# Performance work log

Hardware: AMD Instinct MI355X
Metric: run time of the kernel (lower is better)

The kernel has to match this reference:

```python
import jax, jax.numpy as jnp
import numpy as np

B, S, D = 8, 1024, 1024
H, DK, DV = 16, 64, 64
LN_EPS = 1e-5
NEG = -1.0e9


def setup_inputs() -> dict:
    key = jax.random.key(0)
    k1, k2, k3, k4, k5, k6, k7 = jax.random.split(key, 7)
    sc = 0.02
    input_Q = jax.random.normal(k1, (B, S, D), dtype=jnp.float32)
    input_K = jax.random.normal(k2, (B, S, D), dtype=jnp.float32)
    input_V = jax.random.normal(k3, (B, S, D), dtype=jnp.float32)
    # causal mask: True = masked (as in torch masked_fill_)
    attn_mask = jnp.broadcast_to(jnp.triu(jnp.ones((S, S), dtype=bool), k=1), (B, S, S))
    Wq = jax.random.normal(k4, (D, H * DK), dtype=jnp.float32) * sc
    Wk = jax.random.normal(k5, (D, H * DK), dtype=jnp.float32) * sc
    Wv = jax.random.normal(k6, (D, H * DV), dtype=jnp.float32) * sc
    Wfc = jax.random.normal(k7, (H * DV, D), dtype=jnp.float32) * sc
    return {"input_Q": input_Q, "input_K": input_K, "input_V": input_V,
            "attn_mask": attn_mask, "Wq": Wq, "Wk": Wk, "Wv": Wv, "Wfc": Wfc}


def _layernorm(x):
    mu = jnp.mean(x, axis=-1, keepdims=True)
    var = jnp.var(x, axis=-1, keepdims=True)
    return (x - mu) * jax.lax.rsqrt(var + LN_EPS)  # gamma=1, beta=0 (fresh nn.LayerNorm)


def reference(input_Q, input_K, input_V, attn_mask, Wq, Wk, Wv, Wfc):
    residual = input_Q
    # project and split heads: [B,S,H*dk] -> [B,H,S,dk]
    Q = (input_Q @ Wq).reshape(B, S, H, DK).transpose(0, 2, 1, 3)
    K = (input_K @ Wk).reshape(B, S, H, DK).transpose(0, 2, 1, 3)
    V = (input_V @ Wv).reshape(B, S, H, DV).transpose(0, 2, 1, 3)
    scores = jnp.einsum('bhqd,bhkd->bhqk', Q, K) / np.sqrt(DK).astype(np.float32)
    scores = jnp.where(attn_mask[:, None, :, :], NEG, scores)
    attn = jax.nn.softmax(scores, axis=-1)            # [B,H,S,S]
    context = jnp.einsum('bhqk,bhkd->bhqd', attn, V)  # [B,H,S,dv]
    context = context.transpose(0, 2, 1, 3).reshape(B, S, H * DV)
    out = _layernorm(residual + context @ Wfc)        # [B,S,D]
    return out, attn
```

## Files before the change

### kernel.cpp

```cpp
#include <hip/hip_runtime.h>
#include <hip/hip_bf16.h>

#define BB 8
#define SS 1024
#define DD 1024
#define HH 16
#define DKK 64
#define MM (BB*SS)
#define OUT_ELEMS ((size_t)BB*SS*DD)
#define ATTN_ELEMS ((size_t)BB*HH*SS*SS)

using short8 = __attribute__((ext_vector_type(8))) short;
using f32x4  = __attribute__((ext_vector_type(4))) float;

__device__ __forceinline__ ushort f2b(float f) {
    unsigned u = __float_as_uint(f);
    u = u + 0x7fffu + ((u >> 16) & 1u);
    return (ushort)(u >> 16);
}

__global__ __launch_bounds__(256) void transpose_w(
    const float* __restrict__ w0, const float* __restrict__ w1,
    const float* __restrict__ w2, const float* __restrict__ w3,
    ushort* __restrict__ t0, ushort* __restrict__ t1,
    ushort* __restrict__ t2, ushort* __restrict__ t3)
{
    const float* W; ushort* T;
    switch (blockIdx.z) {
        case 0: W = w0; T = t0; break;
        case 1: W = w1; T = t1; break;
        case 2: W = w2; T = t2; break;
        default: W = w3; T = t3; break;
    }
    __shared__ float tile[64 * 65];
    const int k0 = blockIdx.x * 64, n0 = blockIdx.y * 64;
    const int t = threadIdx.x;
#pragma unroll
    for (int i = 0; i < 16; i++) {
        int idx = i * 256 + t;
        int r = idx >> 6, c = idx & 63;
        tile[r * 65 + c] = W[(size_t)(k0 + r) * DD + n0 + c];
    }
    __syncthreads();
#pragma unroll
    for (int i = 0; i < 16; i++) {
        int idx = i * 256 + t;
        int nr = idx >> 6, kc = idx & 63;
        T[(size_t)(n0 + nr) * DD + k0 + kc] = f2b(tile[kc * 65 + nr]);
    }
}

template <int MODE>
__global__ __launch_bounds__(256) void gemm_bt(
    const float* __restrict__ A, const ushort* __restrict__ Bt,
    void* __restrict__ Cout)
{
    constexpr int K = 1024;
    const int t = threadIdx.x;
    const int n0 = blockIdx.x * 128, m0 = blockIdx.y * 128;
    const int lane = t & 63, w = t >> 6;
    const int li = lane & 15, quad = lane >> 4;
    const int wm = w >> 1, wn = w & 1;

    __shared__ ushort As[128 * 40];

    f32x4 acc[4][4];
    const f32x4 zf = {0.f, 0.f, 0.f, 0.f};
#pragma unroll
    for (int mf = 0; mf < 4; mf++)
#pragma unroll
        for (int nf = 0; nf < 4; nf++) acc[mf][nf] = zf;

    for (int kk = 0; kk < K; kk += 32) {
        __syncthreads();
#pragma unroll
        for (int i = 0; i < 4; i++) {
            int row = (t >> 3) + i * 32;
            float4 a4 = *(const float4*)&A[(size_t)(m0 + row) * K + kk + (t & 7) * 4];
            ushort4 u4 = make_ushort4(f2b(a4.x), f2b(a4.y), f2b(a4.z), f2b(a4.w));
            *(ushort4*)&As[row * 40 + (t & 7) * 4] = u4;
        }
        __syncthreads();

        short8 af[4], bf[4];
#pragma unroll
        for (int mf = 0; mf < 4; mf++)
            af[mf] = *(const short8*)&As[(wm * 64 + mf * 16 + li) * 40 + quad * 8];
#pragma unroll
        for (int nf = 0; nf < 4; nf++)
            bf[nf] = *(const short8*)&Bt[(size_t)(n0 + wn * 64 + nf * 16 + li) * K + kk + quad * 8];
#pragma unroll
        for (int mf = 0; mf < 4; mf++)
#pragma unroll
            for (int nf = 0; nf < 4; nf++)
                acc[mf][nf] = __builtin_amdgcn_mfma_f32_16x16x32_bf16(af[mf], bf[nf], acc[mf][nf], 0, 0, 0);
    }

#pragma unroll
    for (int mf = 0; mf < 4; mf++)
#pragma unroll
        for (int nf = 0; nf < 4; nf++)
#pragma unroll
            for (int r = 0; r < 4; r++) {
                int m = m0 + wm * 64 + mf * 16 + quad * 4 + r;
                int n = n0 + wn * 64 + nf * 16 + li;
                float v = acc[mf][nf][r];
                if (MODE == 0) {
                    int b = m >> 10, s = m & 1023, h = n >> 6, d = n & 63;
                    ((ushort*)Cout)[((size_t)(b * HH + h) * SS + s) * 64 + d] = f2b(v);
                } else if (MODE == 1) {
                    int b = m >> 10, s = m & 1023, h = n >> 6, d = n & 63;
                    ((ushort*)Cout)[((size_t)(b * HH + h) * 64 + d) * SS + s] = f2b(v);
                } else {
                    ((float*)Cout)[(size_t)m * 1024 + n] = v;
                }
            }
}

__global__ __launch_bounds__(256) void attn_kernel(
    const ushort* __restrict__ Qp, const ushort* __restrict__ Kp,
    const ushort* __restrict__ VpT, float* __restrict__ attn,
    float* __restrict__ Ctx)
{
    const int qt = blockIdx.x;
    const int h  = blockIdx.y;
    const int b  = blockIdx.z;
    const int bh = b * HH + h;
    const int t = threadIdx.x;
    const int w = t >> 6, lane = t & 63;
    const int li = lane & 15, quad = lane >> 4;
    const int qbase = qt * 64 + w * 16;

    const ushort* Qh = Qp  + (size_t)bh * SS * 64;
    const ushort* Kh = Kp  + (size_t)bh * SS * 64;
    const ushort* Vt = VpT + (size_t)bh * 64 * SS;
    float* arow = attn + (size_t)bh * SS * SS;

    __shared__ ushort Ps[4][16 * 32];
    ushort* myP = Ps[w];

    short8 aq0 = *(const short8*)&Qh[(size_t)(qbase + li) * 64 + quad * 8];
    short8 aq1 = *(const short8*)&Qh[(size_t)(qbase + li) * 64 + 32 + quad * 8];

    const f32x4 zf = {0.f, 0.f, 0.f, 0.f};
    float lsum[4] = {0.f, 0.f, 0.f, 0.f};
    f32x4 cacc[4];
#pragma unroll
    for (int vf = 0; vf < 4; vf++) cacc[vf] = zf;

    const int nch = (qt + 1) * 2;

    for (int c = 0; c < nch; c++) {
        const int kb = c * 32;
#pragma unroll
        for (int half = 0; half < 2; half++) {
            const int col = kb + half * 16 + li;
            short8 bk0 = *(const short8*)&Kh[(size_t)col * 64 + quad * 8];
            short8 bk1 = *(const short8*)&Kh[(size_t)col * 64 + 32 + quad * 8];
            f32x4 s = __builtin_amdgcn_mfma_f32_16x16x32_bf16(aq0, bk0, zf, 0, 0, 0);
            s = __builtin_amdgcn_mfma_f32_16x16x32_bf16(aq1, bk1, s, 0, 0, 0);
#pragma unroll
            for (int r = 0; r < 4; r++) {
                const int row = qbase + quad * 4 + r;
                float p = (col <= row) ? __expf(s[r] * 0.125f) : 0.f;
                lsum[r] += p;
                myP[(quad * 4 + r) * 32 + half * 16 + li] = f2b(p);
            }
        }
        __syncthreads();
        short8 ap = *(const short8*)&myP[li * 32 + quad * 8];
#pragma unroll
        for (int vf = 0; vf < 4; vf++) {
            short8 bv = *(const short8*)&Vt[(size_t)(vf * 16 + li) * SS + kb + quad * 8];
            cacc[vf] = __builtin_amdgcn_mfma_f32_16x16x32_bf16(ap, bv, cacc[vf], 0, 0, 0);
        }
        __syncthreads();
    }

#pragma unroll
    for (int r = 0; r < 4; r++) {
        float v = lsum[r];
        v += __shfl_xor(v, 1, 64);
        v += __shfl_xor(v, 2, 64);
        v += __shfl_xor(v, 4, 64);
        v += __shfl_xor(v, 8, 64);
        lsum[r] = 1.f / v;
    }

#pragma unroll
    for (int vf = 0; vf < 4; vf++)
#pragma unroll
        for (int r = 0; r < 4; r++) {
            const int s_idx = qbase + quad * 4 + r;
            Ctx[((size_t)b * SS + s_idx) * DD + h * 64 + vf * 16 + li] = cacc[vf][r] * lsum[r];
        }

    for (int c16 = 0; c16 < SS / 16; c16++) {
        const int kb = c16 * 16;
        const int col = kb + li;
        if (kb > qbase + 15) {
#pragma unroll
            for (int r = 0; r < 4; r++)
                arow[(size_t)(qbase + quad * 4 + r) * SS + col] = 0.f;
        } else {
            short8 bk0 = *(const short8*)&Kh[(size_t)col * 64 + quad * 8];
            short8 bk1 = *(const short8*)&Kh[(size_t)col * 64 + 32 + quad * 8];
            f32x4 s = __builtin_amdgcn_mfma_f32_16x16x32_bf16(aq0, bk0, zf, 0, 0, 0);
            s = __builtin_amdgcn_mfma_f32_16x16x32_bf16(aq1, bk1, s, 0, 0, 0);
#pragma unroll
            for (int r = 0; r < 4; r++) {
                const int row = qbase + quad * 4 + r;
                float p = (col <= row) ? __expf(s[r] * 0.125f) * lsum[r] : 0.f;
                arow[(size_t)row * SS + col] = p;
            }
        }
    }
}

__global__ __launch_bounds__(256) void ln_kernel(
    const float* __restrict__ res, float* __restrict__ io)
{
    const int row = blockIdx.x;
    const int t = threadIdx.x;
    float4 p4 = *(const float4*)&io[(size_t)row * DD + t * 4];
    float4 r4 = *(const float4*)&res[(size_t)row * DD + t * 4];
    float x0 = p4.x + r4.x, x1 = p4.y + r4.y, x2 = p4.z + r4.z, x3 = p4.w + r4.w;
    float s  = x0 + x1 + x2 + x3;
    float ss = x0 * x0 + x1 * x1 + x2 * x2 + x3 * x3;
#pragma unroll
    for (int m = 1; m < 64; m <<= 1) {
        s  += __shfl_xor(s, m, 64);
        ss += __shfl_xor(ss, m, 64);
    }
    __shared__ float red[8];
    const int w = t >> 6, lane = t & 63;
    if (lane == 0) { red[w] = s; red[4 + w] = ss; }
    __syncthreads();
    if (t == 0) {
        float S1 = red[0] + red[1] + red[2] + red[3];
        float S2 = red[4] + red[5] + red[6] + red[7];
        float mu = S1 * (1.f / 1024.f);
        float var = S2 * (1.f / 1024.f) - mu * mu;
        red[0] = mu;
        red[1] = rsqrtf(var + 1e-5f);
    }
    __syncthreads();
    float mu = red[0], rs = red[1];
    float4 o;
    o.x = (x0 - mu) * rs; o.y = (x1 - mu) * rs;
    o.z = (x2 - mu) * rs; o.w = (x3 - mu) * rs;
    *(float4*)&io[(size_t)row * DD + t * 4] = o;
}

extern "C" void kernel_launch(void* const* d_in, const int* in_sizes, int n_in,
                              void* d_out, int out_size, void* d_ws, size_t ws_size,
                              hipStream_t stream)
{
    const float* Xq  = (const float*)d_in[0];
    const float* Xk  = (const float*)d_in[1];
    const float* Xv  = (const float*)d_in[2];
    const float* Wq  = (const float*)d_in[4];
    const float* Wk  = (const float*)d_in[5];
    const float* Wv  = (const float*)d_in[6];
    const float* Wfc = (const float*)d_in[7];

    char* ws = (char*)d_ws;
    ushort* Wt0 = (ushort*)ws;
    ushort* Wt1 = Wt0 + (size_t)1024 * 1024;
    ushort* Wt2 = Wt1 + (size_t)1024 * 1024;
    ushort* Wt3 = Wt2 + (size_t)1024 * 1024;
    ushort* Qp  = (ushort*)(ws + ((size_t)8  << 20));
    ushort* Kp  = (ushort*)(ws + ((size_t)24 << 20));
    ushort* VpT = (ushort*)(ws + ((size_t)40 << 20));
    float*  Ctx = (float*) (ws + ((size_t)56 << 20));

    float* outp = (float*)d_out;
    float* attn = outp + OUT_ELEMS;

    transpose_w<<<dim3(16, 16, 4), 256, 0, stream>>>(Wq, Wk, Wv, Wfc, Wt0, Wt1, Wt2, Wt3);
    gemm_bt<0><<<dim3(8, 64), 256, 0, stream>>>(Xq, Wt0, Qp);
    gemm_bt<0><<<dim3(8, 64), 256, 0, stream>>>(Xk, Wt1, Kp);
    gemm_bt<1><<<dim3(8, 64), 256, 0, stream>>>(Xv, Wt2, VpT);
    attn_kernel<<<dim3(16, 16, 8), 256, 0, stream>>>(Qp, Kp, VpT, attn, Ctx);
    gemm_bt<2><<<dim3(8, 64), 256, 0, stream>>>(Ctx, Wt3, outp);
    ln_kernel<<<MM, 256, 0, stream>>>(Xq, outp);
}
```

Baseline: 1.233 ms.

## Split attention into balanced PV pass and parallel probability-write pass

The attention kernel is split in two. The first kernel pairs query tile qt with tile 15-qt so that every block does the same amount of causal work. It computes the context and stores the inverse row sums. The second kernel recomputes the scores and writes normalized probabilities over twice as many blocks, using vectorized stores to zero the masked region. The change also replaces per-wave __syncthreads with compiler barriers and remaps GEMM block indices with an XCD-aware swizzle. The cost is recomputing QK^T in the write pass plus an extra launch.

```diff
diff --git a/kernel.cpp b/kernel.cpp
--- a/kernel.cpp
+++ b/kernel.cpp
@@ -57,7 +57,9 @@
 {
     constexpr int K = 1024;
     const int t = threadIdx.x;
-    const int n0 = blockIdx.x * 128, m0 = blockIdx.y * 128;
+    const int wg = blockIdx.x;
+    const int l  = (wg & 7) * 64 + (wg >> 3);
+    const int n0 = (l & 7) * 128, m0 = (l >> 3) * 128;
     const int lane = t & 63, w = t >> 6;
     const int li = lane & 15, quad = lane >> 4;
     const int wm = w >> 1, wn = w & 1;
@@ -117,101 +119,143 @@
             }
 }
 
-__global__ __launch_bounds__(256) void attn_kernel(
+__global__ __launch_bounds__(256) void attn_pv(
     const ushort* __restrict__ Qp, const ushort* __restrict__ Kp,
-    const ushort* __restrict__ VpT, float* __restrict__ attn,
+    const ushort* __restrict__ VpT, float* __restrict__ Invs,
     float* __restrict__ Ctx)
 {
-    const int qt = blockIdx.x;
+    const int pr = blockIdx.x;
     const int h  = blockIdx.y;
     const int b  = blockIdx.z;
     const int bh = b * HH + h;
     const int t = threadIdx.x;
     const int w = t >> 6, lane = t & 63;
     const int li = lane & 15, quad = lane >> 4;
-    const int qbase = qt * 64 + w * 16;
 
     const ushort* Qh = Qp  + (size_t)bh * SS * 64;
     const ushort* Kh = Kp  + (size_t)bh * SS * 64;
     const ushort* Vt = VpT + (size_t)bh * 64 * SS;
-    float* arow = attn + (size_t)bh * SS * SS;
 
     __shared__ ushort Ps[4][16 * 32];
     ushort* myP = Ps[w];
+    const f32x4 zf = {0.f, 0.f, 0.f, 0.f};
+
+    for (int sel = 0; sel < 2; sel++) {
+        const int qt = sel ? (15 - pr) : pr;
+        const int qbase = qt * 64 + w * 16;
+
+        short8 aq0 = *(const short8*)&Qh[(size_t)(qbase + li) * 64 + quad * 8];
+        short8 aq1 = *(const short8*)&Qh[(size_t)(qbase + li) * 64 + 32 + quad * 8];
+
+        float lsum[4] = {0.f, 0.f, 0.f, 0.f};
+        f32x4 cacc[4];
+#pragma unroll
+        for (int vf = 0; vf < 4; vf++) cacc[vf] = zf;
+
+        const int nch = (qt + 1) * 2;
+
+        for (int c = 0; c < nch; c++) {
+            const int kb = c * 32;
+#pragma unroll
+            for (int half = 0; half < 2; half++) {
+                const int col = kb + half * 16 + li;
+                short8 bk0 = *(const short8*)&Kh[(size_t)col * 64 + quad * 8];
+                short8 bk1 = *(const short8*)&Kh[(size_t)col * 64 + 32 + quad * 8];
+                f32x4 s = __builtin_amdgcn_mfma_f32_16x16x32_bf16(aq0, bk0, zf, 0, 0, 0);
+                s = __builtin_amdgcn_mfma_f32_16x16x32_bf16(aq1, bk1, s, 0, 0, 0);
+#pragma unroll
+                for (int r = 0; r < 4; r++) {
+                    const int row = qbase + quad * 4 + r;
+                    float p = (col <= row) ? __expf(s[r] * 0.125f) : 0.f;
+                    lsum[r] += p;
+                    myP[(quad * 4 + r) * 32 + half * 16 + li] = f2b(p);
+                }
+            }
+            asm volatile("" ::: "memory");
+            short8 ap = *(const short8*)&myP[li * 32 + quad * 8];
+#pragma unroll
+            for (int vf = 0; vf < 4; vf++) {
+                short8 bv = *(const short8*)&Vt[(size_t)(vf * 16 + li) * SS + kb + quad * 8];
+                cacc[vf] = __builtin_amdgcn_mfma_f32_16x16x32_bf16(ap, bv, cacc[vf], 0, 0, 0);
+            }
+            asm volatile("" ::: "memory");
+        }
+
+#pragma unroll
+        for (int r = 0; r < 4; r++) {
+            float v = lsum[r];
+            v += __shfl_xor(v, 1, 64);
+            v += __shfl_xor(v, 2, 64);
+            v += __shfl_xor(v, 4, 64);
+            v += __shfl_xor(v, 8, 64);
+            lsum[r] = 1.f / v;
+        }
+        if (li == 0) {
+#pragma unroll
+            for (int r = 0; r < 4; r++)
+                Invs[(size_t)bh * SS + qbase + quad * 4 + r] = lsum[r];
+        }
+
+#pragma unroll
+        for (int vf = 0; vf < 4; vf++)
+#pragma unroll
+            for (int r = 0; r < 4; r++) {
+                const int s_idx = qbase + quad * 4 + r;
+                Ctx[((size_t)b * SS + s_idx) * DD + h * 64 + vf * 16 + li] = cacc[vf][r] * lsum[r];
+            }
+    }
+}
+
+__global__ __launch_bounds__(256) void attn_write(
+    const ushort* __restrict__ Qp, const ushort* __restrict__ Kp,
+    const float* __restrict__ Invs, float* __restrict__ attn)
+{
+    const int qt = blockIdx.x >> 1;
+    const int ch = blockIdx.x & 1;
+    const int h  = blockIdx.y;
+    const int b  = blockIdx.z;
+    const int bh = b * HH + h;
+    const int t = threadIdx.x;
+    const int w = t >> 6, lane = t & 63;
+    const int li = lane & 15, quad = lane >> 4;
+    const int qbase = qt * 64 + w * 16;
+    const int c0 = ch * 512;
+
+    const ushort* Qh = Qp + (size_t)bh * SS * 64;
+    const ushort* Kh = Kp + (size_t)bh * SS * 64;
+    float* arow = attn + (size_t)bh * SS * SS;
+
+    const f32x4 zf = {0.f, 0.f, 0.f, 0.f};
 
     short8 aq0 = *(const short8*)&Qh[(size_t)(qbase + li) * 64 + quad * 8];
     short8 aq1 = *(const short8*)&Qh[(size_t)(qbase + li) * 64 + 32 + quad * 8];
-
-    const f32x4 zf = {0.f, 0.f, 0.f, 0.f};
-    float lsum[4] = {0.f, 0.f, 0.f, 0.f};
-    f32x4 cacc[4];
-#pragma unroll
-    for (int vf = 0; vf < 4; vf++) cacc[vf] = zf;
-
-    const int nch = (qt + 1) * 2;
-
-    for (int c = 0; c < nch; c++) {
-        const int kb = c * 32;
-#pragma unroll
-        for (int half = 0; half < 2; half++) {
-            const int col = kb + half * 16 + li;
-            short8 bk0 = *(const short8*)&Kh[(size_t)col * 64 + quad * 8];
-            short8 bk1 = *(const short8*)&Kh[(size_t)col * 64 + 32 + quad * 8];
-            f32x4 s = __builtin_amdgcn_mfma_f32_16x16x32_bf16(aq0, bk0, zf, 0, 0, 0);
-            s = __builtin_amdgcn_mfma_f32_16x16x32_bf16(aq1, bk1, s, 0, 0, 0);
+    float inv[4];
+#pragma unroll
+    for (int r = 0; r < 4; r++)
+        inv[r] = Invs[(size_t)bh * SS + qbase + quad * 4 + r];
+
+    for (int c64 = 0; c64 < 8; c64++) {
+        const int kb = c0 + c64 * 64;
+        if (kb > qbase + 15) {
 #pragma unroll
             for (int r = 0; r < 4; r++) {
                 const int row = qbase + quad * 4 + r;
-                float p = (col <= row) ? __expf(s[r] * 0.125f) : 0.f;
-                lsum[r] += p;
-                myP[(quad * 4 + r) * 32 + half * 16 + li] = f2b(p);
-            }
-        }
-        __syncthreads();
-        short8 ap = *(const short8*)&myP[li * 32 + quad * 8];
-#pragma unroll
-        for (int vf = 0; vf < 4; vf++) {
-            short8 bv = *(const short8*)&Vt[(size_t)(vf * 16 + li) * SS + kb + quad * 8];
-            cacc[vf] = __builtin_amdgcn_mfma_f32_16x16x32_bf16(ap, bv, cacc[vf], 0, 0, 0);
-        }
-        __syncthreads();
-    }
-
-#pragma unroll
-    for (int r = 0; r < 4; r++) {
-        float v = lsum[r];
-        v += __shfl_xor(v, 1, 64);
-        v += __shfl_xor(v, 2, 64);
-        v += __shfl_xor(v, 4, 64);
-        v += __shfl_xor(v, 8, 64);
-        lsum[r] = 1.f / v;
-    }
-
-#pragma unroll
-    for (int vf = 0; vf < 4; vf++)
-#pragma unroll
-        for (int r = 0; r < 4; r++) {
-            const int s_idx = qbase + quad * 4 + r;
-            Ctx[((size_t)b * SS + s_idx) * DD + h * 64 + vf * 16 + li] = cacc[vf][r] * lsum[r];
-        }
-
-    for (int c16 = 0; c16 < SS / 16; c16++) {
-        const int kb = c16 * 16;
-        const int col = kb + li;
-        if (kb > qbase + 15) {
-#pragma unroll
-            for (int r = 0; r < 4; r++)
-                arow[(size_t)(qbase + quad * 4 + r) * SS + col] = 0.f;
+                *(f32x4*)&arow[(size_t)row * SS + kb + li * 4] = zf;
+            }
         } else {
-            short8 bk0 = *(const short8*)&Kh[(size_t)col * 64 + quad * 8];
-            short8 bk1 = *(const short8*)&Kh[(size_t)col * 64 + 32 + quad * 8];
-            f32x4 s = __builtin_amdgcn_mfma_f32_16x16x32_bf16(aq0, bk0, zf, 0, 0, 0);
-            s = __builtin_amdgcn_mfma_f32_16x16x32_bf16(aq1, bk1, s, 0, 0, 0);
-#pragma unroll
-            for (int r = 0; r < 4; r++) {
-                const int row = qbase + quad * 4 + r;
-                float p = (col <= row) ? __expf(s[r] * 0.125f) * lsum[r] : 0.f;
-                arow[(size_t)row * SS + col] = p;
+#pragma unroll
+            for (int q16 = 0; q16 < 4; q16++) {
+                const int col = kb + q16 * 16 + li;
+                short8 bk0 = *(const short8*)&Kh[(size_t)col * 64 + quad * 8];
+                short8 bk1 = *(const short8*)&Kh[(size_t)col * 64 + 32 + quad * 8];
+                f32x4 s = __builtin_amdgcn_mfma_f32_16x16x32_bf16(aq0, bk0, zf, 0, 0, 0);
+                s = __builtin_amdgcn_mfma_f32_16x16x32_bf16(aq1, bk1, s, 0, 0, 0);
+#pragma unroll
+                for (int r = 0; r < 4; r++) {
+                    const int row = qbase + quad * 4 + r;
+                    float p = (col <= row) ? __expf(s[r] * 0.125f) * inv[r] : 0.f;
+                    arow[(size_t)row * SS + col] = p;
+                }
             }
         }
     }
@@ -273,15 +317,17 @@
     ushort* Kp  = (ushort*)(ws + ((size_t)24 << 20));
     ushort* VpT = (ushort*)(ws + ((size_t)40 << 20));
     float*  Ctx = (float*) (ws + ((size_t)56 << 20));
+    float*  Invs = (float*)ws;
 
     float* outp = (float*)d_out;
     float* attn = outp + OUT_ELEMS;
 
     transpose_w<<<dim3(16, 16, 4), 256, 0, stream>>>(Wq, Wk, Wv, Wfc, Wt0, Wt1, Wt2, Wt3);
-    gemm_bt<0><<<dim3(8, 64), 256, 0, stream>>>(Xq, Wt0, Qp);
-    gemm_bt<0><<<dim3(8, 64), 256, 0, stream>>>(Xk, Wt1, Kp);
-    gemm_bt<1><<<dim3(8, 64), 256, 0, stream>>>(Xv, Wt2, VpT);
-    attn_kernel<<<dim3(16, 16, 8), 256, 0, stream>>>(Qp, Kp, VpT, attn, Ctx);
-    gemm_bt<2><<<dim3(8, 64), 256, 0, stream>>>(Ctx, Wt3, outp);
+    gemm_bt<0><<<dim3(512), 256, 0, stream>>>(Xq, Wt0, Qp);
+    gemm_bt<0><<<dim3(512), 256, 0, stream>>>(Xk, Wt1, Kp);
+    gemm_bt<1><<<dim3(512), 256, 0, stream>>>(Xv, Wt2, VpT);
+    attn_pv<<<dim3(8, 16, 8), 256, 0, stream>>>(Qp, Kp, VpT, Invs, Ctx);
+    attn_write<<<dim3(32, 16, 8), 256, 0, stream>>>(Qp, Kp, Invs, attn);
+    gemm_bt<2><<<dim3(512), 256, 0, stream>>>(Ctx, Wt3, outp);
     ln_kernel<<<MM, 256, 0, stream>>>(Xq, outp);
 }
```

New measurement: 1.158 ms. 6.1% less time.
